# Optimization experiments

Hardware: AMD Instinct MI355X
Metric: run time of the kernel (lower is better)

## Reference

```python
import jax, jax.numpy as jnp
import numpy as np

TEMPERATURE = 0.75
SINKHORN_ITERS = 7
EPS = 1e-6
R_THRESH = 1e-3


def setup_inputs() -> dict:
    key = jax.random.key(0)
    k1, k2, k3, k4 = jax.random.split(key, 4)
    b, h, t, d = 1, 8, 2048, 64
    n = 32  # uniform buckets of size t // n = 64
    q = jax.random.normal(k1, (b, h, t, d), jnp.float32)
    k_ = jax.random.normal(k2, (b, h, t, d), jnp.float32)
    v = jax.random.normal(k3, (b, h, t, d), jnp.float32)
    gumbel_u = jax.random.uniform(k4, (b * h, n, n), jnp.float32)
    return {"q": q, "k": k_, "v": v, "gumbel_u": gumbel_u, "num_buckets": n}


def _sort_net_R(qm, km, gumbel_u, d):
    # qm, km: [bh, n, s, d] -> bucket sums [bh, n, d]
    q_sums = qm.sum(axis=2)
    k_sums = km.sum(axis=2)
    logits = jnp.einsum('bie,bje->bij', q_sums, k_sums) * (d ** -0.5)
    # gumbel_sinkhorn(relu(logits))
    r = jnp.log(jax.nn.relu(logits) + EPS)
    g = -jnp.log(-jnp.log(gumbel_u + EPS) + EPS)
    r = (r + g) / TEMPERATURE
    for _ in range(SINKHORN_ITERS):
        r = r - jax.nn.logsumexp(r, axis=2, keepdims=True)
        r = r - jax.nn.logsumexp(r, axis=1, keepdims=True)
    return jnp.exp(r)  # [bh, n, n]


def reference(q, k, v, gumbel_u, num_buckets):
    b, h, t, d = q.shape
    bh = b * h
    n = num_buckets
    s = t // n  # uniform bucket size
    qm = q.reshape(bh, n, s, d)
    km = k.reshape(bh, n, s, d)
    vm = v.reshape(bh, n, s, d)

    R = _sort_net_R(qm, km, gumbel_u, d)
    # torch skips pairs with R_ij <= 1e-3 (output is zero); multiply by masked R
    Rm = jnp.where(R > R_THRESH, R, 0.0)

    scale = d ** -0.5
    # keys for pair (i, j) are concat(k_i, k_j): split score into self + cross
    S_self = jnp.einsum('bise,bite->bist', qm, km) * scale          # [bh,n,s,s]
    S_cross = jnp.einsum('bise,bjte->bijst', qm, km) * scale        # [bh,n,n,s,s]
    scores = jnp.concatenate(
        [jnp.broadcast_to(S_self[:, :, None], (bh, n, n, s, s)), S_cross],
        axis=-1)                                                    # [bh,n,n,s,2s]
    w = jax.nn.softmax(scores, axis=-1)
    w_i, w_j = w[..., :s], w[..., s:]
    # out_ij = (w_i @ v_i + w_j @ v_j) * R_ij, summed over j
    out = (jnp.einsum('bijst,bite,bij->bise', w_i, vm, Rm)
           + jnp.einsum('bijst,bjte,bij->bise', w_j, vm, Rm))       # [bh,n,s,d]
    return out.reshape(b, h, t, d)
```

## Files before the change

### kernel.cpp

```cpp
#include <hip/hip_runtime.h>
#include <math.h>
#include <stdint.h>

#define BH 8
#define NB 32
#define SS 64
#define DD 64
#define TT 2048

typedef float f32x16 __attribute__((ext_vector_type(16)));
typedef short bf16x8 __attribute__((ext_vector_type(8)));
typedef unsigned short u16;

__device__ __forceinline__ unsigned pkbf(float a, float b) {
  unsigned r;
  asm("v_cvt_pk_bf16_f32 %0, %1, %2" : "=v"(r) : "v"(a), "v"(b));
  return r;
}
__device__ __forceinline__ float exp2x(float x) {
  float r;
  asm("v_exp_f32 %0, %1" : "=v"(r) : "v"(x));
  return r;
}
__device__ __forceinline__ float log2x(float x) {
  float r;
  asm("v_log_f32 %0, %1" : "=v"(r) : "v"(x));
  return r;
}
__device__ __forceinline__ bf16x8 pack8v(const f32x16& v, const int b) {
  union { unsigned u[4]; bf16x8 v8; } x;
  x.u[0] = pkbf(v[b + 0], v[b + 1]);
  x.u[1] = pkbf(v[b + 2], v[b + 3]);
  x.u[2] = pkbf(v[b + 4], v[b + 5]);
  x.u[3] = pkbf(v[b + 6], v[b + 7]);
  return x.v8;
}

__global__ __launch_bounds__(256) void prep_kernel(
    const float* __restrict__ q, const float* __restrict__ k, const float* __restrict__ v,
    u16* __restrict__ qb, u16* __restrict__ kb, u16* __restrict__ vtb,
    float* __restrict__ qsum, float* __restrict__ ksum)
{
  __shared__ float qt[64][68];
  __shared__ float kt[64][68];
  __shared__ float vt[64][68];

  const int T = blockIdx.x;
  const int t = threadIdx.x;
  const float* qsrc = q + (size_t)T * 4096;
  const float* ksrc = k + (size_t)T * 4096;
  const float* vsrc = v + (size_t)T * 4096;

#pragma unroll
  for (int r4 = 0; r4 < 4; ++r4) {
    int f = r4 * 256 + t;
    int row = f >> 4, c4 = (f & 15) << 2;
    *(float4*)&qt[row][c4] = ((const float4*)qsrc)[f];
    *(float4*)&kt[row][c4] = ((const float4*)ksrc)[f];
    *(float4*)&vt[row][c4] = ((const float4*)vsrc)[f];
  }
  __syncthreads();

  const float qscale = 0.18033688011112042f;

#pragma unroll
  for (int half = 0; half < 2; ++half) {
    int x = half * 256 + t;
    int c = x >> 6, lane = x & 63;
    int l31 = lane & 31, hi = lane >> 5;
    int m = c >> 2, s = c & 3;
    int row = l31 + 32 * m;
    int cb = 16 * s + 4 * hi;
    float4 a = *(const float4*)&qt[row][cb];
    float4 b = *(const float4*)&qt[row][cb + 8];
    uint4 o;
    o.x = pkbf(a.x * qscale, a.y * qscale);
    o.y = pkbf(a.z * qscale, a.w * qscale);
    o.z = pkbf(b.x * qscale, b.y * qscale);
    o.w = pkbf(b.z * qscale, b.w * qscale);
    *(uint4*)(qb + (size_t)T * 4096 + (size_t)x * 8) = o;

    float4 ka = *(const float4*)&kt[row][cb];
    float4 kb4 = *(const float4*)&kt[row][cb + 8];
    uint4 ko;
    ko.x = pkbf(ka.x, ka.y);
    ko.y = pkbf(ka.z, ka.w);
    ko.z = pkbf(kb4.x, kb4.y);
    ko.w = pkbf(kb4.z, kb4.w);
    *(uint4*)(kb + (size_t)T * 4096 + (size_t)x * 8) = ko;

    int d = l31 + 32 * m;
    int kb0 = 16 * s + 4 * hi;
    uint4 vo;
    vo.x = pkbf(vt[kb0 + 0][d], vt[kb0 + 1][d]);
    vo.y = pkbf(vt[kb0 + 2][d], vt[kb0 + 3][d]);
    vo.z = pkbf(vt[kb0 + 8][d], vt[kb0 + 9][d]);
    vo.w = pkbf(vt[kb0 + 10][d], vt[kb0 + 11][d]);
    *(uint4*)(vtb + (size_t)T * 4096 + (size_t)x * 8) = vo;
  }

  if (t < 64) {
    float s = 0.f;
#pragma unroll 8
    for (int r = 0; r < 64; ++r) s += qt[r][t];
    qsum[T * 64 + t] = s;
  } else if (t < 128) {
    int c = t - 64;
    float s = 0.f;
#pragma unroll 8
    for (int r = 0; r < 64; ++r) s += kt[r][c];
    ksum[T * 64 + c] = s;
  }
}

__global__ __launch_bounds__(512) void attn_kernel(
    const u16* __restrict__ qb, const u16* __restrict__ kb,
    const u16* __restrict__ vtb, const float* __restrict__ qsum,
    const float* __restrict__ ksum, const float* __restrict__ gu,
    float* __restrict__ out)
{
  __shared__ __align__(16) unsigned char smem[131072];
  float (*redh)[2][32][68] = (float (*)[2][32][68])smem;
  float (*cbuf)[32] = (float (*)[32])(smem + 34816);

  const int bh  = blockIdx.x & 7;
  const int i   = blockIdx.x >> 3;
  const int t   = threadIdx.x;
  const int w   = t >> 6;
  const int n   = w & 1;
  const int g   = w >> 1;
  const int lane = t & 63;
  const int l31 = lane & 31;
  const int hi  = lane >> 5;

  const u16* qtile = qb + ((size_t)(bh * NB + i)) * 4096;
  const u16* kbh   = kb + (size_t)bh * NB * 4096;
  const u16* vbh   = vtb + (size_t)bh * NB * 4096;

#define GLDS(srcp, dstp)                                                      \
  __builtin_amdgcn_global_load_lds(                                           \
      (const __attribute__((address_space(1))) void*)(srcp),                  \
      (__attribute__((address_space(3))) void*)(dstp), 16, 0, 0)

#define STAGE(p, r)                                                           \
  {                                                                           \
    const u16* srcT = (w < 4) ? (kbh + (size_t)(w + 4 * (r)) * 4096)          \
                              : (vbh + (size_t)(w - 4 + 4 * (r)) * 4096);     \
    unsigned char* dstT = smem + (p) * 65536 + w * 8192;                      \
    _Pragma("unroll") for (int ii = 0; ii < 8; ++ii)                          \
      GLDS(srcT + (size_t)(ii * 64 + lane) * 8, dstT + ii * 1024);            \
  }

#define LOADL(dst, p, tile)                                                   \
  {                                                                           \
    const u16* baseL = (const u16*)(smem + (p) * 65536 + (tile) * 8192);      \
    _Pragma("unroll") for (int m = 0; m < 2; ++m)                             \
    _Pragma("unroll") for (int s = 0; s < 4; ++s)                             \
      dst[m][s] = *(const bf16x8*)(baseL + ((m * 4 + s) * 64 + lane) * 8);    \
  }

#define LOADG(dst, base)                                                      \
  {                                                                           \
    _Pragma("unroll") for (int m = 0; m < 2; ++m)                             \
    _Pragma("unroll") for (int s = 0; s < 4; ++s)                             \
      dst[m][s] = *(const bf16x8*)((base) + ((size_t)((m * 4 + s) * 64 + lane)) * 8); \
  }

  STAGE(0, 0);

  bf16x8 qB[4];
#pragma unroll
  for (int s = 0; s < 4; ++s)
    qB[s] = *(const bf16x8*)(qtile + ((size_t)((n * 4 + s) * 64 + lane)) * 8);

  float rij8[8];
  {
    const float L2E = 1.4426950408889634f;
    const float LN2 = 0.6931471805599453f;
    float* qs    = (float*)(smem + 65536);
    float* ks    = qs + 32 * 65;
    float* rbufS = ks + 32 * 65;
    float* colb  = rbufS + 32 * 33;
    float* RmRow = colb + 32;

    {
      int idx = t * 4;
      float4 qv = *(const float4*)(qsum + bh * 2048 + idx);
      float4 kv = *(const float4*)(ksum + bh * 2048 + idx);
      int b = idx >> 6, e = idx & 63;
      float* qd = qs + b * 65 + e;
      qd[0] = qv.x; qd[1] = qv.y; qd[2] = qv.z; qd[3] = qv.w;
      float* kd = ks + b * 65 + e;
      kd[0] = kv.x; kd[1] = kv.y; kd[2] = kv.z; kd[3] = kv.w;
    }
    __syncthreads();

    const int G = t >> 5;
    const int j = t & 31;
    float rr2[2];
#pragma unroll
    for (int x = 0; x < 2; ++x) {
      int ii = G + 16 * x;
      float acc = 0.f;
      for (int e = 0; e < 64; ++e) acc += qs[ii * 65 + e] * ks[j * 65 + e];
      acc *= 0.125f;
      float u = gu[bh * 1024 + ii * 32 + j];
      float gg = -logf(-logf(u + 1e-6f) + 1e-6f);
      rr2[x] = (logf(fmaxf(acc, 0.f) + 1e-6f) + gg) * (1.0f / 0.75f);
    }

    for (int it = 0; it < 7; ++it) {
#pragma unroll
      for (int x = 0; x < 2; ++x) {
        float s = exp2x(rr2[x] * L2E);
        s += __shfl_xor(s, 16, 32);
        s += __shfl_xor(s, 8, 32);
        s += __shfl_xor(s, 4, 32);
        s += __shfl_xor(s, 2, 32);
        s += __shfl_xor(s, 1, 32);
        rr2[x] -= log2x(fmaxf(s, 1e-30f)) * LN2;
      }
#pragma unroll
      for (int x = 0; x < 2; ++x) rbufS[(G + 16 * x) * 33 + j] = rr2[x];
      __syncthreads();
#pragma unroll
      for (int x = 0; x < 2; ++x) {
        int col = G + 16 * x;
        float s2 = exp2x(rbufS[j * 33 + col] * L2E);
        s2 += __shfl_xor(s2, 16, 32);
        s2 += __shfl_xor(s2, 8, 32);
        s2 += __shfl_xor(s2, 4, 32);
        s2 += __shfl_xor(s2, 2, 32);
        s2 += __shfl_xor(s2, 1, 32);
        if (j == 0) colb[col] = log2x(fmaxf(s2, 1e-30f)) * LN2;
      }
      __syncthreads();
#pragma unroll
      for (int x = 0; x < 2; ++x) rr2[x] -= colb[j];
    }

#pragma unroll
    for (int x = 0; x < 2; ++x) {
      if (G + 16 * x == i) {
        float R = exp2x(rr2[x] * L2E);
        RmRow[j] = (R > 1e-3f) ? R : 0.f;
      }
    }
    __syncthreads();
#pragma unroll
    for (int jj = 0; jj < 8; ++jj) rij8[jj] = RmRow[g + 4 * jj];
  }

  float m0, S0;
  bf16x8 psA[4];
  {
    const u16* kib = kbh + (size_t)i * 4096;
    bf16x8 kAi[2][4];
    LOADG(kAi, kib);
    f32x16 aS0, aS1;
#pragma unroll
    for (int r = 0; r < 16; ++r) { aS0[r] = 0.f; aS1[r] = 0.f; }
#pragma unroll
    for (int s = 0; s < 4; ++s) {
      aS0 = __builtin_amdgcn_mfma_f32_32x32x16_bf16(kAi[0][s], qB[s], aS0, 0, 0, 0);
      aS1 = __builtin_amdgcn_mfma_f32_32x32x16_bf16(kAi[1][s], qB[s], aS1, 0, 0, 0);
    }
    float mx[16];
#pragma unroll
    for (int r = 0; r < 16; ++r) mx[r] = fmaxf(aS0[r], aS1[r]);
#pragma unroll
    for (int off = 8; off > 0; off >>= 1)
#pragma unroll
      for (int r = 0; r < off; ++r) mx[r] = fmaxf(mx[r], mx[r + off]);
    float mm = fmaxf(mx[0], __shfl_xor(mx[0], 32, 64));
#pragma unroll
    for (int r = 0; r < 16; ++r) { aS0[r] = exp2x(aS0[r] - mm); aS1[r] = exp2x(aS1[r] - mm); }
    float sm[16];
#pragma unroll
    for (int r = 0; r < 16; ++r) sm[r] = aS0[r] + aS1[r];
#pragma unroll
    for (int off = 8; off > 0; off >>= 1)
#pragma unroll
      for (int r = 0; r < off; ++r) sm[r] += sm[r + off];
    S0 = sm[0] + __shfl_xor(sm[0], 32, 64);
    m0 = mm;
    psA[0] = pack8v(aS0, 0);
    psA[1] = pack8v(aS0, 8);
    psA[2] = pack8v(aS1, 0);
    psA[3] = pack8v(aS1, 8);
  }

  f32x16 outAcc[2];
#pragma unroll
  for (int nv = 0; nv < 2; ++nv)
#pragma unroll
    for (int e = 0; e < 16; ++e) outAcc[nv][e] = 0.f;
  float cacc = 0.f;

#pragma unroll
  for (int rr = 0; rr < 8; ++rr) {
    const int p = rr & 1;
    asm volatile("s_waitcnt vmcnt(0)" ::: "memory");
    __builtin_amdgcn_s_barrier();
    __builtin_amdgcn_sched_barrier(0);
    if (rr < 7) STAGE(p ^ 1, rr + 1);

    const float rij = rij8[rr];
    bf16x8 kA[2][4], vB[2][4];
    LOADL(kA, p, g);
    LOADL(vB, p, 4 + g);

    f32x16 a0, a1;
#pragma unroll
    for (int r = 0; r < 16; ++r) { a0[r] = 0.f; a1[r] = 0.f; }
    __builtin_amdgcn_s_setprio(1);
#pragma unroll
    for (int s = 0; s < 4; ++s) {
      a0 = __builtin_amdgcn_mfma_f32_32x32x16_bf16(kA[0][s], qB[s], a0, 0, 0, 0);
      a1 = __builtin_amdgcn_mfma_f32_32x32x16_bf16(kA[1][s], qB[s], a1, 0, 0, 0);
    }
    __builtin_amdgcn_s_setprio(0);

    float mx[16];
#pragma unroll
    for (int r = 0; r < 16; ++r) mx[r] = fmaxf(a0[r], a1[r]);
#pragma unroll
    for (int off = 8; off > 0; off >>= 1)
#pragma unroll
      for (int r = 0; r < off; ++r) mx[r] = fmaxf(mx[r], mx[r + off]);
    float mc = fmaxf(mx[0], __shfl_xor(mx[0], 32, 64));
    float mj = fmaxf(m0, mc);
#pragma unroll
    for (int r = 0; r < 16; ++r) { a0[r] = exp2x(a0[r] - mj); a1[r] = exp2x(a1[r] - mj); }
    float sm[16];
#pragma unroll
    for (int r = 0; r < 16; ++r) sm[r] = a0[r] + a1[r];
#pragma unroll
    for (int off = 8; off > 0; off >>= 1)
#pragma unroll
      for (int r = 0; r < off; ++r) sm[r] += sm[r + off];
    float ssum = sm[0] + __shfl_xor(sm[0], 32, 64);
    float e0 = exp2x(m0 - mj);
    float den = S0 * e0 + ssum;
    float inv = rij / den;
    cacc += e0 * inv;
#pragma unroll
    for (int r = 0; r < 16; ++r) { a0[r] *= inv; a1[r] *= inv; }

    __builtin_amdgcn_s_setprio(1);
#pragma unroll
    for (int s = 0; s < 4; ++s) {
      bf16x8 wf = (s < 2) ? pack8v(a0, 8 * (s & 1)) : pack8v(a1, 8 * (s & 1));
      outAcc[0] = __builtin_amdgcn_mfma_f32_32x32x16_bf16(wf, vB[0][s], outAcc[0], 0, 0, 0);
      outAcc[1] = __builtin_amdgcn_mfma_f32_32x32x16_bf16(wf, vB[1][s], outAcc[1], 0, 0, 0);
    }
    __builtin_amdgcn_s_setprio(0);
  }

  {
    const u16* vib = vbh + (size_t)i * 4096;
    bf16x8 vBi[2][4];
    LOADG(vBi, vib);
    f32x16 U[2];
#pragma unroll
    for (int nv = 0; nv < 2; ++nv)
#pragma unroll
      for (int e = 0; e < 16; ++e) U[nv][e] = 0.f;
#pragma unroll
    for (int s = 0; s < 4; ++s) {
      U[0] = __builtin_amdgcn_mfma_f32_32x32x16_bf16(psA[s], vBi[0][s], U[0], 0, 0, 0);
      U[1] = __builtin_amdgcn_mfma_f32_32x32x16_bf16(psA[s], vBi[1][s], U[1], 0, 0, 0);
    }
    if (hi == 0) cbuf[w][l31] = cacc;
    __syncthreads();
#pragma unroll
    for (int r = 0; r < 16; ++r) {
      int row = (r & 3) + 8 * (r >> 2) + 4 * hi;
      float cr = cbuf[w][row];
      outAcc[0][r] += U[0][r] * cr;
      outAcc[1][r] += U[1][r] * cr;
    }
  }

#define RED_W(buf)                                                         \
  {                                                                        \
    _Pragma("unroll") for (int ne = 0; ne < 2; ++ne)                       \
    _Pragma("unroll") for (int r = 0; r < 16; ++r) {                       \
      int row = (r & 3) + 8 * (r >> 2) + 4 * hi;                           \
      (buf)[row][l31 + 32 * ne] = outAcc[ne][r];                           \
    }                                                                      \
  }
#define RED_A(buf)                                                         \
  {                                                                        \
    _Pragma("unroll") for (int ne = 0; ne < 2; ++ne)                       \
    _Pragma("unroll") for (int r = 0; r < 16; ++r) {                       \
      int row = (r & 3) + 8 * (r >> 2) + 4 * hi;                           \
      outAcc[ne][r] += (buf)[row][l31 + 32 * ne];                          \
    }                                                                      \
  }

  if (g >= 2) RED_W(redh[n][g - 2]);
  __syncthreads();
  if (g < 2) RED_A(redh[n][g]);
  __syncthreads();
  if (g == 1) RED_W(redh[n][0]);
  __syncthreads();
  if (g == 0) {
    RED_A(redh[n][0]);
    RED_W(redh[n][0]);
  }
  __syncthreads();

  {
    int row = t >> 3;
    int nr = row >> 5, lrow = row & 31;
    int col0 = (t & 7) * 8;
    float4 a = *(const float4*)&redh[nr][0][lrow][col0];
    float4 b = *(const float4*)&redh[nr][0][lrow][col0 + 4];
    float* ob = out + ((size_t)bh * TT + i * SS + row) * DD + col0;
    *(float4*)ob = a;
    *(float4*)(ob + 4) = b;
  }
#undef GLDS
#undef STAGE
#undef LOADL
#undef LOADG
#undef RED_W
#undef RED_A
}

extern "C" void kernel_launch(void* const* d_in, const int* in_sizes, int n_in,
                              void* d_out, int out_size, void* d_ws, size_t ws_size,
                              hipStream_t stream) {
  (void)in_sizes; (void)n_in; (void)out_size; (void)ws_size;
  const float* q  = (const float*)d_in[0];
  const float* k  = (const float*)d_in[1];
  const float* v  = (const float*)d_in[2];
  const float* gu = (const float*)d_in[3];
  float* out = (float*)d_out;

  char* wsb = (char*)d_ws;
  u16* qb   = (u16*)(wsb);
  u16* kb   = (u16*)(wsb + (1 << 21));
  u16* vtb  = (u16*)(wsb + (2 << 21));
  float* qsum = (float*)(wsb + (3 << 21));
  float* ksum = (float*)(wsb + (3 << 21) + (1 << 16));

  prep_kernel<<<256, 256, 0, stream>>>(q, k, v, qb, kb, vtb, qsum, ksum);
  attn_kernel<<<BH * NB, 512, 0, stream>>>(qb, kb, vtb, qsum, ksum, gu, out);
}
```

Measured before the change: 36.41 us.

## Replace LDS double-buffered K/V staging with direct register global loads

```diff
diff --git a/kernel.cpp b/kernel.cpp
--- a/kernel.cpp
+++ b/kernel.cpp
@@ -119,9 +119,14 @@
     const float* __restrict__ ksum, const float* __restrict__ gu,
     float* __restrict__ out)
 {
-  __shared__ __align__(16) unsigned char smem[131072];
+  __shared__ __align__(16) unsigned char smem[35840];
   float (*redh)[2][32][68] = (float (*)[2][32][68])smem;
   float (*cbuf)[32] = (float (*)[32])(smem + 34816);
+  float* qs    = (float*)smem;
+  float* ks    = qs + 32 * 65;
+  float* rbufS = ks + 32 * 65;
+  float* colb  = rbufS + 32 * 33;
+  float* RmRow = colb + 32;
 
   const int bh  = blockIdx.x & 7;
   const int i   = blockIdx.x >> 3;
@@ -137,28 +142,6 @@
   const u16* kbh   = kb + (size_t)bh * NB * 4096;
   const u16* vbh   = vtb + (size_t)bh * NB * 4096;
 
-#define GLDS(srcp, dstp)                                                      \
-  __builtin_amdgcn_global_load_lds(                                           \
-      (const __attribute__((address_space(1))) void*)(srcp),                  \
-      (__attribute__((address_space(3))) void*)(dstp), 16, 0, 0)
-
-#define STAGE(p, r)                                                           \
-  {                                                                           \
-    const u16* srcT = (w < 4) ? (kbh + (size_t)(w + 4 * (r)) * 4096)          \
-                              : (vbh + (size_t)(w - 4 + 4 * (r)) * 4096);     \
-    unsigned char* dstT = smem + (p) * 65536 + w * 8192;                      \
-    _Pragma("unroll") for (int ii = 0; ii < 8; ++ii)                          \
-      GLDS(srcT + (size_t)(ii * 64 + lane) * 8, dstT + ii * 1024);            \
-  }
-
-#define LOADL(dst, p, tile)                                                   \
-  {                                                                           \
-    const u16* baseL = (const u16*)(smem + (p) * 65536 + (tile) * 8192);      \
-    _Pragma("unroll") for (int m = 0; m < 2; ++m)                             \
-    _Pragma("unroll") for (int s = 0; s < 4; ++s)                             \
-      dst[m][s] = *(const bf16x8*)(baseL + ((m * 4 + s) * 64 + lane) * 8);    \
-  }
-
 #define LOADG(dst, base)                                                      \
   {                                                                           \
     _Pragma("unroll") for (int m = 0; m < 2; ++m)                             \
@@ -166,8 +149,6 @@
       dst[m][s] = *(const bf16x8*)((base) + ((size_t)((m * 4 + s) * 64 + lane)) * 8); \
   }
 
-  STAGE(0, 0);
-
   bf16x8 qB[4];
 #pragma unroll
   for (int s = 0; s < 4; ++s)
@@ -177,11 +158,6 @@
   {
     const float L2E = 1.4426950408889634f;
     const float LN2 = 0.6931471805599453f;
-    float* qs    = (float*)(smem + 65536);
-    float* ks    = qs + 32 * 65;
-    float* rbufS = ks + 32 * 65;
-    float* colb  = rbufS + 32 * 33;
-    float* RmRow = colb + 32;
 
     {
       int idx = t * 4;
@@ -251,6 +227,10 @@
     for (int jj = 0; jj < 8; ++jj) rij8[jj] = RmRow[g + 4 * jj];
   }
 
+  bf16x8 kA[2][4], vB[2][4];
+  LOADG(kA, kbh + (size_t)g * 4096);
+  LOADG(vB, vbh + (size_t)g * 4096);
+
   float m0, S0;
   bf16x8 psA[4];
   {
@@ -298,17 +278,9 @@
   float cacc = 0.f;
 
 #pragma unroll
-  for (int rr = 0; rr < 8; ++rr) {
-    const int p = rr & 1;
-    asm volatile("s_waitcnt vmcnt(0)" ::: "memory");
-    __builtin_amdgcn_s_barrier();
-    __builtin_amdgcn_sched_barrier(0);
-    if (rr < 7) STAGE(p ^ 1, rr + 1);
-
-    const float rij = rij8[rr];
-    bf16x8 kA[2][4], vB[2][4];
-    LOADL(kA, p, g);
-    LOADL(vB, p, 4 + g);
+  for (int jj = 0; jj < 8; ++jj) {
+    const int j = g + 4 * jj;
+    const float rij = rij8[jj];
 
     f32x16 a0, a1;
 #pragma unroll
@@ -320,6 +292,8 @@
       a1 = __builtin_amdgcn_mfma_f32_32x32x16_bf16(kA[1][s], qB[s], a1, 0, 0, 0);
     }
     __builtin_amdgcn_s_setprio(0);
+
+    if (jj < 7) LOADG(kA, kbh + (size_t)(j + 4) * 4096);
 
     float mx[16];
 #pragma unroll
@@ -355,6 +329,8 @@
       outAcc[1] = __builtin_amdgcn_mfma_f32_32x32x16_bf16(wf, vB[1][s], outAcc[1], 0, 0, 0);
     }
     __builtin_amdgcn_s_setprio(0);
+
+    if (jj < 7) LOADG(vB, vbh + (size_t)(j + 4) * 4096);
   }
 
   {
@@ -421,9 +397,6 @@
     *(float4*)ob = a;
     *(float4*)(ob + 4) = b;
   }
-#undef GLDS
-#undef STAGE
-#undef LOADL
 #undef LOADG
 #undef RED_W
 #undef RED_A
```

Measured after the change: 34.26 us. 5.9% less time.
